# Performance work log

Measured on AMD Instinct MI355X. Metric: run time of the kernel, lower is better.

## Reference

```python
import jax, jax.numpy as jnp
import numpy as np

INPUT_DIM = 6
HIDDEN = 128


def neighbor_mean(x, adj):
    # x: [B,N,F], adj: [B,N,N]; node i averages itself + neighbors (adj>0)
    mask = (adj > 0).astype(x.dtype)  # [B,N,N]
    s = jnp.einsum('bij,bjf->bif', mask, x) + x  # sum neighbors + self
    cnt = mask.sum(-1) + 1.0  # [B,N]
    return s / cnt[..., None]


def lstm_scan(x, Wi, Wh, bi, bh, reverse=False):
    # x: [B,T,F]; Wi: [4H,F]; Wh: [4H,H]; gate order i,f,g,o (torch)
    B, T, F = x.shape
    H = Wh.shape[1]
    xw = jnp.einsum('btf,gf->btg', x, Wi) + bi + bh  # [B,T,4H]
    def step(carry, xt):
        h, c = carry
        z = xt + h @ Wh.T  # [B,4H]
        i, f, g, o = jnp.split(z, 4, axis=-1)
        i = jax.nn.sigmoid(i); f = jax.nn.sigmoid(f)
        g = jnp.tanh(g); o = jax.nn.sigmoid(o)
        c = f * c + i * g
        h = o * jnp.tanh(c)
        return (h, c), h
    init = (jnp.zeros((B, H), x.dtype), jnp.zeros((B, H), x.dtype))
    xs = jnp.swapaxes(xw, 0, 1)  # [T,B,4H]
    (hT, cT), hs = jax.lax.scan(step, init, xs, reverse=reverse)
    return hT


def setup_inputs():
    key = jax.random.key(0)
    ks = jax.random.split(key, 12)
    B, N = 4096, 64
    inp = {
        'device_idx': jax.random.uniform(ks[0], (B,), jnp.float32),
        'matrix': jax.random.uniform(ks[1], (B, N, N), jnp.float32),
        'features': jax.random.normal(ks[2], (B, N, INPUT_DIM), jnp.float32),
    }
    s = 1.0 / np.sqrt(HIDDEN)
    def u(k, shape):
        return jax.random.uniform(k, shape, jnp.float32, -s, s)
    inp['Wi_f'] = u(ks[3], (4 * HIDDEN, INPUT_DIM))
    inp['Wh_f'] = u(ks[4], (4 * HIDDEN, HIDDEN))
    inp['bi_f'] = u(ks[5], (4 * HIDDEN,))
    inp['bh_f'] = u(ks[6], (4 * HIDDEN,))
    inp['Wi_b'] = u(ks[7], (4 * HIDDEN, INPUT_DIM))
    inp['Wh_b'] = u(ks[8], (4 * HIDDEN, HIDDEN))
    inp['bi_b'] = u(ks[9], (4 * HIDDEN,))
    inp['bh_b'] = u(ks[10], (4 * HIDDEN,))
    inp['fc_w'] = u(ks[11], (1, 2 * HIDDEN + 1))
    inp['fc_b'] = jnp.zeros((1,), jnp.float32)
    return inp


def reference(device_idx, matrix, features, Wi_f, Wh_f, bi_f, bh_f, Wi_b, Wh_b, bi_b, bh_b, fc_w, fc_b):
    upd = neighbor_mean(features, matrix)  # [B,N,6]
    h_fwd = lstm_scan(upd, Wi_f, Wh_f, bi_f, bh_f, reverse=False)  # [B,H]
    h_bwd = lstm_scan(upd, Wi_b, Wh_b, bi_b, bh_b, reverse=True)   # [B,H]
    hn = jnp.concatenate([h_fwd, h_bwd], axis=1)  # [B,2H]
    final = jnp.concatenate([device_idx[:, None], hn], axis=1)  # [B,2H+1]
    y = final @ fc_w.T + fc_b
    return y.reshape(-1)
```

## Files before the change

kernel.cpp:

```cpp
#include <hip/hip_runtime.h>
#include <hip/hip_bf16.h>

#define B_TOTAL 4096
#define LOG2E 1.44269504088896f

typedef short short8 __attribute__((ext_vector_type(8)));
typedef float f32x4 __attribute__((ext_vector_type(4)));
typedef float f32x2 __attribute__((ext_vector_type(2)));
typedef int   i32x4 __attribute__((ext_vector_type(4)));

__device__ __forceinline__ unsigned short rne_bf16(float x) {
    unsigned int u = __float_as_uint(x);
    unsigned int r = (u + 0x7fffu + ((u >> 16) & 1u)) >> 16;
    return (unsigned short)r;
}
__device__ __forceinline__ unsigned int cvt2bf(float lo, float hi) {
    unsigned int r;
    asm("v_cvt_pk_bf16_f32 %0, %1, %2" : "=v"(r) : "v"(lo), "v"(hi));
    return r;
}
__device__ __forceinline__ f32x2 v2(float x) { f32x2 r; r[0] = x; r[1] = x; return r; }

__global__ __launch_bounds__(256) void k_neighbor_mean(
    const float* __restrict__ matrix,
    const float* __restrict__ features,
    float* __restrict__ upd)
{
    __shared__ float adj[64][65];
    __shared__ float fx[64][6];
    const int b = blockIdx.x;
    const int tid = threadIdx.x;
    const float* mb_ = matrix + (size_t)b * 4096;
    for (int idx = tid; idx < 4096; idx += 256) adj[idx >> 6][idx & 63] = mb_[idx];
    const float* fb = features + (size_t)b * 384;
    for (int idx = tid; idx < 384; idx += 256) fx[idx / 6][idx % 6] = fb[idx];
    __syncthreads();
    if (tid < 64) {
        const int i = tid;
        float s0=0,s1=0,s2=0,s3=0,s4=0,s5=0,cnt=0;
        for (int j = 0; j < 64; j++) {
            float m = adj[i][j] > 0.0f ? 1.0f : 0.0f;
            cnt += m;
            s0 += m*fx[j][0]; s1 += m*fx[j][1]; s2 += m*fx[j][2];
            s3 += m*fx[j][3]; s4 += m*fx[j][4]; s5 += m*fx[j][5];
        }
        const float inv = 1.0f / (cnt + 1.0f);
        float* o = upd + (size_t)b * 384 + i * 6;
        o[0]=(s0+fx[i][0])*inv; o[1]=(s1+fx[i][1])*inv; o[2]=(s2+fx[i][2])*inv;
        o[3]=(s3+fx[i][3])*inv; o[4]=(s4+fx[i][4])*inv; o[5]=(s5+fx[i][5])*inv;
    }
}

__global__ __launch_bounds__(256) void k_wprep5(
    const float* __restrict__ Wi_f, const float* __restrict__ Wh_f,
    const float* __restrict__ bi_f, const float* __restrict__ bh_f,
    const float* __restrict__ Wi_b, const float* __restrict__ Wh_b,
    const float* __restrict__ bi_b, const float* __restrict__ bh_b,
    signed char* __restrict__ Wd1, signed char* __restrict__ Wd2,
    unsigned short* __restrict__ AwU, float* __restrict__ BqO)
{
    const int idx = blockIdx.x * 256 + threadIdx.x;
    if (idx < 131072) {
        const int dir = idx >> 16;
        const int r = idx & 65535;
        const int mtg = r >> 11;
        const int kc  = (r >> 10) & 1;
        const int l   = (r >> 4) & 63;
        const int e   = r & 15;
        const int n = mtg * 16 + (l & 15);
        const int j = ((n & 3) << 7) + (n >> 2);
        const int ks = kc * 64 + 16 * (l >> 4) + e;
        const int hu = 8 * (ks >> 3) + 4 * (ks & 1) + ((ks & 7) >> 1);
        const float w = (dir ? Wh_b : Wh_f)[j * 128 + hu];
        const float a = w * (512.0f * LOG2E);
        const float r1 = rintf(a);
        Wd1[idx] = (signed char)(int)r1;
        Wd2[idx] = (signed char)(int)rintf((a - r1) * 128.0f);
    } else if (idx < 163840) {
        const int i2 = idx - 131072;
        const int dir = i2 >> 14;
        const int r = i2 & 16383;
        const int mtg = r >> 9, l = (r >> 3) & 63, e = r & 7;
        const int n = mtg * 16 + (l & 15);
        const int j = ((n & 3) << 7) + (n >> 2);
        const float sc = ((n & 3) == 2) ? 2.0f * LOG2E : LOG2E;
        float w = 0.0f;
        if ((l >> 4) == 0 && e < 6) w = (dir ? Wi_b : Wi_f)[j * 6 + e] * sc;
        AwU[i2] = rne_bf16(w);
    } else if (idx < 164864) {
        const int i2 = idx - 163840;
        const int dir = i2 >> 9;
        const int n = i2 & 511;
        const int j = ((n & 3) << 7) + (n >> 2);
        const float sc = ((n & 3) == 2) ? 2.0f * LOG2E : LOG2E;
        BqO[i2] = ((dir ? bi_b : bi_f)[j] + (dir ? bh_b : bh_f)[j]) * sc;
    }
}

__global__ __launch_bounds__(1024) void k_lstm12(
    const float* __restrict__ upd,
    const signed char* __restrict__ Wd1,
    const signed char* __restrict__ Wd2,
    const unsigned short* __restrict__ AwU,
    const float* __restrict__ Bq,
    float* __restrict__ hout)
{
    __shared__ i32x4 HsV[2048];
    __shared__ i32x4 UsV[2048];
    char* Hb = (char*)HsV;
    char* Ub = (char*)UsV;
    const int tid  = threadIdx.x;
    const int wave = tid >> 6;
    const int lane = tid & 63;
    const int dir  = blockIdx.y;
    const int b0   = blockIdx.x * 32;
    const int l15  = lane & 15;
    const int lhi  = lane >> 4;
    const int hu0  = 8 * wave + lhi, hu1 = hu0 + 4;
    const bool issueFirst = ((wave >> 2) & 1) != 0;

    i32x4 wd1[2][2], wd2[2][2];
    short8 awu[2];
    f32x4 bias[2];
    #pragma unroll
    for (int mt = 0; mt < 2; mt++) {
        const int mtg = 2 * wave + mt;
        #pragma unroll
        for (int kc = 0; kc < 2; kc++) {
            wd1[mt][kc] = *(const i32x4*)(Wd1 + dir * 65536 + mtg * 2048 + kc * 1024 + lane * 16);
            wd2[mt][kc] = *(const i32x4*)(Wd2 + dir * 65536 + mtg * 2048 + kc * 1024 + lane * 16);
        }
        awu[mt]  = *(const short8*)(AwU + dir * 16384 + mtg * 512 + lane * 8);
        bias[mt] = *(const f32x4*)(Bq + dir * 512 + mtg * 16 + 4 * lhi);
    }

    for (int i = tid; i < 2048; i += 1024) {
        const int t = i >> 5, b = i & 31;
        const float2* p = (const float2*)(upd + (size_t)(b0 + b) * 384 + t * 6);
        const float2 a0 = p[0], a1 = p[1], a2 = p[2];
        i32x4 v;
        v[0] = (int)cvt2bf(a0.x, a0.y);
        v[1] = (int)cvt2bf(a1.x, a1.y);
        v[2] = (int)cvt2bf(a2.x, a2.y);
        v[3] = 0;
        *(i32x4*)(Ub + (b >> 4) * 16384 + t * 256 + (b & 15) * 16) = v;
    }
    for (int i = tid; i < 8192; i += 1024) ((int*)Hb)[i] = 0;

    int ra[2], wa[2];
    #pragma unroll
    for (int g = 0; g < 2; g++) {
        ra[g] = g * 16384 + 4096 + l15 * 144 + lhi * 16;
        wa[g] = g * 16384 + l15 * 144 + 8 * wave + 2 * lhi;
    }
    f32x2 cs0 = v2(0.0f), cs1 = v2(0.0f);
    f32x4 Ua[2][2];
    i32x4 Aa[2][2], Ba[2][2];
    __syncthreads();

    const i32x4 zi = {0, 0, 0, 0};
    const f32x2 one2 = v2(1.0f);
    const f32x2 two2 = v2(2.0f);

    auto ISSUE = [&](int iv) {
        const int gi = (iv & 1) ^ 1;
        const int si = (iv + 1) >> 1;
        const int tt = dir ? (63 - si) : si;
        const short8 fu = *(const short8*)(Ub + gi * 16384 + tt * 256 + l15 * 16);
        const i32x4 h1k0 = *(const i32x4*)(Hb + ra[gi]);
        const i32x4 h1k1 = *(const i32x4*)(Hb + ra[gi] + 64);
        const i32x4 h2k0 = *(const i32x4*)(Hb + ra[gi] + 8192);
        const i32x4 h2k1 = *(const i32x4*)(Hb + ra[gi] + 8256);
        ra[gi] ^= 0x1000;
        __builtin_amdgcn_s_setprio(1);
        #pragma unroll
        for (int mt = 0; mt < 2; mt++) {
            Ua[gi][mt] = __builtin_amdgcn_mfma_f32_16x16x32_bf16(awu[mt], fu, bias[mt], 0, 0, 0);
            i32x4 a = __builtin_amdgcn_mfma_i32_16x16x64_i8(wd1[mt][0], h1k0, zi, 0, 0, 0);
            a = __builtin_amdgcn_mfma_i32_16x16x64_i8(wd1[mt][1], h1k1, a, 0, 0, 0);
            i32x4 b = __builtin_amdgcn_mfma_i32_16x16x64_i8(wd1[mt][0], h2k0, zi, 0, 0, 0);
            b = __builtin_amdgcn_mfma_i32_16x16x64_i8(wd1[mt][1], h2k1, b, 0, 0, 0);
            b = __builtin_amdgcn_mfma_i32_16x16x64_i8(wd2[mt][0], h1k0, b, 0, 0, 0);
            b = __builtin_amdgcn_mfma_i32_16x16x64_i8(wd2[mt][1], h1k1, b, 0, 0, 0);
            Aa[gi][mt] = a; Ba[gi][mt] = b;
        }
        __builtin_amdgcn_s_setprio(0);
    };

    auto MATH = [&](int gc, int sc) {
        f32x2& cs = gc ? cs1 : cs0;
        f32x2 ex[4];
        #pragma unroll
        for (int g = 0; g < 4; g++) {
            const int T0 = (Aa[gc][0][g] << 7) + Ba[gc][0][g];
            const int T1 = (Aa[gc][1][g] << 7) + Ba[gc][1][g];
            float a0, a1;
            if (g == 2) {
                a0 = fmaf((float)T0,  0x1p-21f,  Ua[gc][0][g]);
                a1 = fmaf((float)T1,  0x1p-21f,  Ua[gc][1][g]);
            } else {
                a0 = fmaf((float)T0, -0x1p-22f, -Ua[gc][0][g]);
                a1 = fmaf((float)T1, -0x1p-22f, -Ua[gc][1][g]);
            }
            ex[g][0] = __builtin_amdgcn_exp2f(a0);
            ex[g][1] = __builtin_amdgcn_exp2f(a1);
        }
        const f32x2 D0 = ex[0] + one2;
        const f32x2 D1 = ex[1] + one2;
        const f32x2 D2 = ex[2] + one2;
        const f32x2 D3 = ex[3] + one2;
        const f32x2 P2 = D0 * D1, P3 = P2 * D2, P4 = P3 * D3;
        const float rall = __builtin_amdgcn_rcpf(P4[0] * P4[1]);
        f32x2 rv;
        rv[0] = rall * P4[1];
        rv[1] = rall * P4[0];
        const f32x2 Q2 = D3 * D2, Q3 = Q2 * D1;
        const f32x2 ig = rv * Q3;
        const f32x2 fg = rv * Q2 * D0;
        const f32x2 og = rv * P3;
        const f32x2 gg = one2 - two2 * (rv * P2 * D3);
        cs = fg * cs + ig * gg;
        const float aa0 = fminf(cs[0] * (2.0f * LOG2E), 30.0f);
        const float aa1 = fminf(cs[1] * (2.0f * LOG2E), 30.0f);
        const float Dq0 = 1.0f + __builtin_amdgcn_exp2f(aa0);
        const float Dq1 = 1.0f + __builtin_amdgcn_exp2f(aa1);
        const float rq = __builtin_amdgcn_rcpf(Dq0 * Dq1);
        const float hh0 = og[0] * fmaf(-2.0f, rq * Dq1, 1.0f);
        const float hh1 = og[1] * fmaf(-2.0f, rq * Dq0, 1.0f);

        if (sc < 63) {
            const int t0 = __float_as_int(fmaf(hh0, 8192.0f, 12582912.0f)) - 0x4B400000;
            const int t1 = __float_as_int(fmaf(hh1, 8192.0f, 12582912.0f)) - 0x4B400000;
            const int d10 = (t0 + 64) >> 7;
            const int d20 = t0 - (d10 << 7);
            const int d11 = (t1 + 64) >> 7;
            const int d21 = t1 - (d11 << 7);
            *(unsigned short*)(Hb + wa[gc]) =
                (unsigned short)__builtin_amdgcn_perm((unsigned)d11, (unsigned)d10, 0x0400);
            *(unsigned short*)(Hb + wa[gc] + 8192) =
                (unsigned short)__builtin_amdgcn_perm((unsigned)d21, (unsigned)d20, 0x0400);
        } else {
            float* o = hout + ((size_t)dir * B_TOTAL + b0 + gc * 16 + l15) * 128;
            o[hu0] = hh0;
            o[hu1] = hh1;
        }
        wa[gc] ^= 0x1000;
    };

    {
        const int tt = dir ? 63 : 0;
        const short8 fu = *(const short8*)(Ub + tt * 256 + l15 * 16);
        const i32x4 h1k0 = *(const i32x4*)(Hb + ra[0]);
        const i32x4 h1k1 = *(const i32x4*)(Hb + ra[0] + 64);
        const i32x4 h2k0 = *(const i32x4*)(Hb + ra[0] + 8192);
        const i32x4 h2k1 = *(const i32x4*)(Hb + ra[0] + 8256);
        ra[0] ^= 0x1000;
        #pragma unroll
        for (int mt = 0; mt < 2; mt++) {
            Ua[0][mt] = __builtin_amdgcn_mfma_f32_16x16x32_bf16(awu[mt], fu, bias[mt], 0, 0, 0);
            i32x4 a = __builtin_amdgcn_mfma_i32_16x16x64_i8(wd1[mt][0], h1k0, zi, 0, 0, 0);
            a = __builtin_amdgcn_mfma_i32_16x16x64_i8(wd1[mt][1], h1k1, a, 0, 0, 0);
            i32x4 b = __builtin_amdgcn_mfma_i32_16x16x64_i8(wd1[mt][0], h2k0, zi, 0, 0, 0);
            b = __builtin_amdgcn_mfma_i32_16x16x64_i8(wd1[mt][1], h2k1, b, 0, 0, 0);
            b = __builtin_amdgcn_mfma_i32_16x16x64_i8(wd2[mt][0], h1k0, b, 0, 0, 0);
            b = __builtin_amdgcn_mfma_i32_16x16x64_i8(wd2[mt][1], h1k1, b, 0, 0, 0);
            Aa[0][mt] = a; Ba[0][mt] = b;
        }
    }

    #pragma unroll 2
    for (int iv = 0; iv < 128; ++iv) {
        const int gc = iv & 1;
        const int sc = iv >> 1;
        if (issueFirst) {
            if (iv < 127) ISSUE(iv);
            MATH(gc, sc);
        } else {
            MATH(gc, sc);
            if (iv < 127) ISSUE(iv);
        }
        __syncthreads();
    }
}

__global__ __launch_bounds__(256) void k_final(
    const float* __restrict__ hout,
    const float* __restrict__ device_idx,
    const float* __restrict__ fc_w,
    const float* __restrict__ fc_b,
    float* __restrict__ y)
{
    const int wave = threadIdx.x >> 6;
    const int lane = threadIdx.x & 63;
    const int b = blockIdx.x * 4 + wave;
    const float* hf = hout + (size_t)b * 128;
    const float* hb = hout + ((size_t)B_TOTAL + b) * 128;
    float p = fc_w[1 + lane]        * hf[lane]
            + fc_w[1 + 64 + lane]   * hf[64 + lane]
            + fc_w[129 + lane]      * hb[lane]
            + fc_w[129 + 64 + lane] * hb[64 + lane];
    #pragma unroll
    for (int off = 32; off; off >>= 1) p += __shfl_xor(p, off, 64);
    if (lane == 0) y[b] = p + fc_w[0] * device_idx[b] + fc_b[0];
}

extern "C" void kernel_launch(void* const* d_in, const int* in_sizes, int n_in,
                              void* d_out, int out_size, void* d_ws, size_t ws_size,
                              hipStream_t stream) {
    const float* device_idx = (const float*)d_in[0];
    const float* matrix     = (const float*)d_in[1];
    const float* features   = (const float*)d_in[2];
    const float* Wi_f = (const float*)d_in[3];
    const float* Wh_f = (const float*)d_in[4];
    const float* bi_f = (const float*)d_in[5];
    const float* bh_f = (const float*)d_in[6];
    const float* Wi_b = (const float*)d_in[7];
    const float* Wh_b = (const float*)d_in[8];
    const float* bi_b = (const float*)d_in[9];
    const float* bh_b = (const float*)d_in[10];
    const float* fc_w = (const float*)d_in[11];
    const float* fc_b = (const float*)d_in[12];
    float* out = (float*)d_out;

    float* ws = (float*)d_ws;
    float*          upd  = ws;
    signed char*    Wd1  = (signed char*)(ws + 1572864);
    signed char*    Wd2  = (signed char*)(ws + 1605632);
    unsigned short* AwU  = (unsigned short*)(ws + 1638400);
    float*          Bq   = ws + 1654784;
    float*          hout = ws + 1655808;

    hipLaunchKernelGGL(k_neighbor_mean, dim3(B_TOTAL), dim3(256), 0, stream,
                       matrix, features, upd);
    hipLaunchKernelGGL(k_wprep5, dim3(644), dim3(256), 0, stream,
                       Wi_f, Wh_f, bi_f, bh_f, Wi_b, Wh_b, bi_b, bh_b,
                       Wd1, Wd2, AwU, Bq);
    hipLaunchKernelGGL(k_lstm12, dim3(B_TOTAL / 32, 2), dim3(1024), 0, stream,
                       upd, Wd1, Wd2, AwU, Bq, hout);
    hipLaunchKernelGGL(k_final, dim3(B_TOTAL / 4), dim3(256), 0, stream,
                       hout, device_idx, fc_w, fc_b, out);
}
```

Baseline: 167.2 us.

## Restructure LSTM step loop: compute cell, issue next MFMAs, then store state

Reorders each recurrent step so every wave computes the gate math, issues the next group's MFMA batch, and only then writes its quantized hidden digits to LDS. This replaces the previous per-wave alternation (issueFirst) and the s_setprio hints. The gate algebra is also simplified to fewer multiplies, using per-element reciprocals and a closed-form cell update. The input-feature LDS address is now an incrementing pointer, and the final two steps are peeled out of the loop. The aim is a shorter dependency chain per step and better MFMA/VALU overlap, at the cost of dropping the staggered wave scheduling and priority hints.

New measurement: 161.1 us. 1.04x faster.

```diff
diff --git a/kernel.cpp b/kernel.cpp
--- a/kernel.cpp
+++ b/kernel.cpp
@@ -97,7 +97,7 @@
     }
 }
 
-__global__ __launch_bounds__(1024) void k_lstm12(
+__global__ __launch_bounds__(1024) void k_lstm13(
     const float* __restrict__ upd,
     const signed char* __restrict__ Wd1,
     const signed char* __restrict__ Wd2,
@@ -117,7 +117,6 @@
     const int l15  = lane & 15;
     const int lhi  = lane >> 4;
     const int hu0  = 8 * wave + lhi, hu1 = hu0 + 4;
-    const bool issueFirst = ((wave >> 2) & 1) != 0;
 
     i32x4 wd1[2][2], wd2[2][2];
     short8 awu[2];
@@ -147,11 +146,13 @@
     }
     for (int i = tid; i < 8192; i += 1024) ((int*)Hb)[i] = 0;
 
-    int ra[2], wa[2];
+    int ra[2], wa[2], ua[2];
+    const int ustride = dir ? -256 : 256;
     #pragma unroll
     for (int g = 0; g < 2; g++) {
         ra[g] = g * 16384 + 4096 + l15 * 144 + lhi * 16;
         wa[g] = g * 16384 + l15 * 144 + 8 * wave + 2 * lhi;
+        ua[g] = g * 16384 + (dir ? 63 * 256 : 0) + l15 * 16;
     }
     f32x2 cs0 = v2(0.0f), cs1 = v2(0.0f);
     f32x4 Ua[2][2];
@@ -160,34 +161,29 @@
 
     const i32x4 zi = {0, 0, 0, 0};
     const f32x2 one2 = v2(1.0f);
-    const f32x2 two2 = v2(2.0f);
-
-    auto ISSUE = [&](int iv) {
-        const int gi = (iv & 1) ^ 1;
-        const int si = (iv + 1) >> 1;
-        const int tt = dir ? (63 - si) : si;
-        const short8 fu = *(const short8*)(Ub + gi * 16384 + tt * 256 + l15 * 16);
-        const i32x4 h1k0 = *(const i32x4*)(Hb + ra[gi]);
-        const i32x4 h1k1 = *(const i32x4*)(Hb + ra[gi] + 64);
-        const i32x4 h2k0 = *(const i32x4*)(Hb + ra[gi] + 8192);
-        const i32x4 h2k1 = *(const i32x4*)(Hb + ra[gi] + 8256);
-        ra[gi] ^= 0x1000;
-        __builtin_amdgcn_s_setprio(1);
+
+    auto ISSUE = [&](int g) {
+        const short8 fu = *(const short8*)(Ub + ua[g]);
+        ua[g] += ustride;
+        const i32x4 h1k0 = *(const i32x4*)(Hb + ra[g]);
+        const i32x4 h1k1 = *(const i32x4*)(Hb + ra[g] + 64);
+        const i32x4 h2k0 = *(const i32x4*)(Hb + ra[g] + 8192);
+        const i32x4 h2k1 = *(const i32x4*)(Hb + ra[g] + 8256);
+        ra[g] ^= 0x1000;
         #pragma unroll
         for (int mt = 0; mt < 2; mt++) {
-            Ua[gi][mt] = __builtin_amdgcn_mfma_f32_16x16x32_bf16(awu[mt], fu, bias[mt], 0, 0, 0);
+            Ua[g][mt] = __builtin_amdgcn_mfma_f32_16x16x32_bf16(awu[mt], fu, bias[mt], 0, 0, 0);
             i32x4 a = __builtin_amdgcn_mfma_i32_16x16x64_i8(wd1[mt][0], h1k0, zi, 0, 0, 0);
             a = __builtin_amdgcn_mfma_i32_16x16x64_i8(wd1[mt][1], h1k1, a, 0, 0, 0);
             i32x4 b = __builtin_amdgcn_mfma_i32_16x16x64_i8(wd1[mt][0], h2k0, zi, 0, 0, 0);
             b = __builtin_amdgcn_mfma_i32_16x16x64_i8(wd1[mt][1], h2k1, b, 0, 0, 0);
             b = __builtin_amdgcn_mfma_i32_16x16x64_i8(wd2[mt][0], h1k0, b, 0, 0, 0);
             b = __builtin_amdgcn_mfma_i32_16x16x64_i8(wd2[mt][1], h1k1, b, 0, 0, 0);
-            Aa[gi][mt] = a; Ba[gi][mt] = b;
+            Aa[g][mt] = a; Ba[g][mt] = b;
         }
-        __builtin_amdgcn_s_setprio(0);
     };
 
-    auto MATH = [&](int gc, int sc) {
+    auto CELL = [&](int gc, float& hh0, float& hh1) {
         f32x2& cs = gc ? cs1 : cs0;
         f32x2 ex[4];
         #pragma unroll
@@ -209,77 +205,65 @@
         const f32x2 D1 = ex[1] + one2;
         const f32x2 D2 = ex[2] + one2;
         const f32x2 D3 = ex[3] + one2;
-        const f32x2 P2 = D0 * D1, P3 = P2 * D2, P4 = P3 * D3;
-        const float rall = __builtin_amdgcn_rcpf(P4[0] * P4[1]);
-        f32x2 rv;
-        rv[0] = rall * P4[1];
-        rv[1] = rall * P4[0];
-        const f32x2 Q2 = D3 * D2, Q3 = Q2 * D1;
-        const f32x2 ig = rv * Q3;
-        const f32x2 fg = rv * Q2 * D0;
-        const f32x2 og = rv * P3;
-        const f32x2 gg = one2 - two2 * (rv * P2 * D3);
-        cs = fg * cs + ig * gg;
+        const f32x2 M  = D0 * D2;
+        const f32x2 M3 = M * D1;
+        const f32x2 M4 = M3 * D3;
+        f32x2 r;
+        r[0] = __builtin_amdgcn_rcpf(M4[0]);
+        r[1] = __builtin_amdgcn_rcpf(M4[1]);
+        const f32x2 rD3 = r * D3;
+        const f32x2 og  = r * M3;
+        const f32x2 t2  = (ex[2] - one2) * D1;
+        cs = (cs * M + t2) * rD3;
         const float aa0 = fminf(cs[0] * (2.0f * LOG2E), 30.0f);
         const float aa1 = fminf(cs[1] * (2.0f * LOG2E), 30.0f);
         const float Dq0 = 1.0f + __builtin_amdgcn_exp2f(aa0);
         const float Dq1 = 1.0f + __builtin_amdgcn_exp2f(aa1);
         const float rq = __builtin_amdgcn_rcpf(Dq0 * Dq1);
-        const float hh0 = og[0] * fmaf(-2.0f, rq * Dq1, 1.0f);
-        const float hh1 = og[1] * fmaf(-2.0f, rq * Dq0, 1.0f);
-
-        if (sc < 63) {
-            const int t0 = __float_as_int(fmaf(hh0, 8192.0f, 12582912.0f)) - 0x4B400000;
-            const int t1 = __float_as_int(fmaf(hh1, 8192.0f, 12582912.0f)) - 0x4B400000;
-            const int d10 = (t0 + 64) >> 7;
-            const int d20 = t0 - (d10 << 7);
-            const int d11 = (t1 + 64) >> 7;
-            const int d21 = t1 - (d11 << 7);
-            *(unsigned short*)(Hb + wa[gc]) =
-                (unsigned short)__builtin_amdgcn_perm((unsigned)d11, (unsigned)d10, 0x0400);
-            *(unsigned short*)(Hb + wa[gc] + 8192) =
-                (unsigned short)__builtin_amdgcn_perm((unsigned)d21, (unsigned)d20, 0x0400);
-        } else {
-            float* o = hout + ((size_t)dir * B_TOTAL + b0 + gc * 16 + l15) * 128;
-            o[hu0] = hh0;
-            o[hu1] = hh1;
-        }
+        hh0 = og[0] * fmaf(-2.0f, rq * Dq1, 1.0f);
+        hh1 = og[1] * fmaf(-2.0f, rq * Dq0, 1.0f);
+    };
+
+    auto STORE_DIGITS = [&](int gc, float hh0, float hh1) {
+        const int t0 = __float_as_int(fmaf(hh0, 8192.0f, 12582912.0f)) - 0x4B400000;
+        const int t1 = __float_as_int(fmaf(hh1, 8192.0f, 12582912.0f)) - 0x4B400000;
+        const int d10 = (t0 + 64) >> 7;
+        const int d20 = t0 - (d10 << 7);
+        const int d11 = (t1 + 64) >> 7;
+        const int d21 = t1 - (d11 << 7);
+        *(unsigned short*)(Hb + wa[gc]) =
+            (unsigned short)__builtin_amdgcn_perm((unsigned)d11, (unsigned)d10, 0x0400);
+        *(unsigned short*)(Hb + wa[gc] + 8192) =
+            (unsigned short)__builtin_amdgcn_perm((unsigned)d21, (unsigned)d20, 0x0400);
         wa[gc] ^= 0x1000;
     };
 
+    ISSUE(0);
+
+    #pragma unroll 2
+    for (int iv = 0; iv < 126; ++iv) {
+        const int gc = iv & 1;
+        float hh0, hh1;
+        CELL(gc, hh0, hh1);
+        ISSUE(gc ^ 1);
+        STORE_DIGITS(gc, hh0, hh1);
+        __syncthreads();
+    }
     {
-        const int tt = dir ? 63 : 0;
-        const short8 fu = *(const short8*)(Ub + tt * 256 + l15 * 16);
-        const i32x4 h1k0 = *(const i32x4*)(Hb + ra[0]);
-        const i32x4 h1k1 = *(const i32x4*)(Hb + ra[0] + 64);
-        const i32x4 h2k0 = *(const i32x4*)(Hb + ra[0] + 8192);
-        const i32x4 h2k1 = *(const i32x4*)(Hb + ra[0] + 8256);
-        ra[0] ^= 0x1000;
-        #pragma unroll
-        for (int mt = 0; mt < 2; mt++) {
-            Ua[0][mt] = __builtin_amdgcn_mfma_f32_16x16x32_bf16(awu[mt], fu, bias[mt], 0, 0, 0);
-            i32x4 a = __builtin_amdgcn_mfma_i32_16x16x64_i8(wd1[mt][0], h1k0, zi, 0, 0, 0);
-            a = __builtin_amdgcn_mfma_i32_16x16x64_i8(wd1[mt][1], h1k1, a, 0, 0, 0);
-            i32x4 b = __builtin_amdgcn_mfma_i32_16x16x64_i8(wd1[mt][0], h2k0, zi, 0, 0, 0);
-            b = __builtin_amdgcn_mfma_i32_16x16x64_i8(wd1[mt][1], h2k1, b, 0, 0, 0);
-            b = __builtin_amdgcn_mfma_i32_16x16x64_i8(wd2[mt][0], h1k0, b, 0, 0, 0);
-            b = __builtin_amdgcn_mfma_i32_16x16x64_i8(wd2[mt][1], h1k1, b, 0, 0, 0);
-            Aa[0][mt] = a; Ba[0][mt] = b;
-        }
-    }
-
-    #pragma unroll 2
-    for (int iv = 0; iv < 128; ++iv) {
-        const int gc = iv & 1;
-        const int sc = iv >> 1;
-        if (issueFirst) {
-            if (iv < 127) ISSUE(iv);
-            MATH(gc, sc);
-        } else {
-            MATH(gc, sc);
-            if (iv < 127) ISSUE(iv);
-        }
+        float hh0, hh1;
+        CELL(0, hh0, hh1);
+        ISSUE(1);
+        float* o = hout + ((size_t)dir * B_TOTAL + b0 + l15) * 128;
+        o[hu0] = hh0;
+        o[hu1] = hh1;
         __syncthreads();
+    }
+    {
+        float hh0, hh1;
+        CELL(1, hh0, hh1);
+        float* o = hout + ((size_t)dir * B_TOTAL + b0 + 16 + l15) * 128;
+        o[hu0] = hh0;
+        o[hu1] = hh1;
     }
 }
 
@@ -335,7 +319,7 @@
     hipLaunchKernelGGL(k_wprep5, dim3(644), dim3(256), 0, stream,
                        Wi_f, Wh_f, bi_f, bh_f, Wi_b, Wh_b, bi_b, bh_b,
                        Wd1, Wd2, AwU, Bq);
-    hipLaunchKernelGGL(k_lstm12, dim3(B_TOTAL / 32, 2), dim3(1024), 0, stream,
+    hipLaunchKernelGGL(k_lstm13, dim3(B_TOTAL / 32, 2), dim3(1024), 0, stream,
                        upd, Wd1, Wd2, AwU, Bq, hout);
     hipLaunchKernelGGL(k_final, dim3(B_TOTAL / 4), dim3(256), 0, stream,
                        hout, device_idx, fc_w, fc_b, out);
```
